# Kernel optimization log

Measured on AMD Instinct MI355X. Metric: run time of the kernel, lower is better.

Reference implementation:

```python
import jax, jax.numpy as jnp
import numpy as np

# normalize2mom(relu): scale so E[act(x)^2] = 1 for x ~ N(0,1). For relu E[relu(x)^2] = 1/2.
ACT_SCALE = 2.0 ** 0.5


def setup_inputs() -> dict:
    key = jax.random.key(0)
    k1, k2, k3 = jax.random.split(key, 3)
    B = 512
    NA, NB = 48, 24          # na = round(2*aspect_ratio*res), nb = 2*res, res=12, ar=2
    DIM = 680                # sum_{l=0}^{7} (2l+1)^2
    features = jax.random.normal(k1, (B, DIM), dtype=jnp.float32)
    D = jax.random.normal(k2, (NA, NB, NA, DIM), dtype=jnp.float32)  # fixed Wigner-D basis buffer
    qw = jax.random.uniform(k3, (NB,), dtype=jnp.float32)            # quadrature weights over beta
    return {"features": features, "D": D, "qw": qw}


def reference(features, D, qw):
    # features: (N, i); D: (a, b, c, i); qw: (b,)
    dim = D.shape[-1]
    inv_sqrt_dim = dim ** -0.5
    # forward SO(3) transform to grid: (N, a, b, c)
    g = jnp.einsum('ni,abci->nabc', features, D) * inv_sqrt_dim
    # pointwise activation (normalized to unit second moment)
    g = ACT_SCALE * jax.nn.relu(g)
    # inverse transform with quadrature weights on the beta axis: (N, i)
    out = jnp.einsum('nabc,abci,b->ni', g, D, qw) * (dim ** 0.5)
    return out
```

## Files before the change

kernel.cpp:

```cpp
#include <hip/hip_runtime.h>

#define BATCH 512
#define SDIM  680
#define DIP   768
#define ABC   55296
#define NB_   24
#define SQRT2F 1.4142135623730951f

typedef __attribute__((ext_vector_type(8))) short bf16x8;
typedef __attribute__((ext_vector_type(4))) float f32x4;

#define DP_BYTES   ((size_t)ABC * DIP * 2)
#define DPT_BYTES  ((size_t)DIP * ABC * 2)
#define FP_BYTES   ((size_t)BATCH * DIP * 2)
#define G_BYTES    ((size_t)BATCH * ABC * 2)
#define DP_OFF     ((size_t)0)
#define DPT_OFF    (DP_OFF + DP_BYTES)
#define FP_OFF     (DPT_OFF + DPT_BYTES)
#define G_OFF      (FP_OFF + FP_BYTES)
#define WS_NEEDED  (G_OFF + G_BYTES)

#define SPLITK 32
#define KC     1728
#define P_OFF  DP_OFF

__device__ __forceinline__ unsigned short f2bf(float f) {
  unsigned int u = __float_as_uint(f);
  unsigned int r = (u + 0x7FFFu + ((u >> 16) & 1u)) >> 16;
  return (unsigned short)r;
}

__device__ __forceinline__ float bf2f(unsigned int bits16) {
  return __uint_as_float(bits16 << 16);
}

__device__ __forceinline__ void stage16(const void* g, const void* l) {
  __builtin_amdgcn_global_load_lds(
      (const __attribute__((address_space(1))) unsigned int*)g,
      (__attribute__((address_space(3))) unsigned int*)l, 16, 0, 0);
}

#define CBP 264
__global__ __launch_bounds__(256) void conv_both(const float* __restrict__ D,
                                                 unsigned short* __restrict__ Dp,
                                                 unsigned short* __restrict__ DpT) {
  __shared__ unsigned short T[64 * CBP];
  const int bid = blockIdx.x;
  const int logical = (bid & 7) * 324 + (bid >> 3);
  const int bx = logical / 12;
  const int by = logical % 12;
  const int t = threadIdx.x;

  #pragma unroll
  for (int k = 0; k < 4; ++k) {
    const int micro = t + k * 256;
    const int r4 = micro >> 4;
    const int c4 = micro & 15;
    const int gr = bx * 256 + r4 * 4;
    const int gi = by * 64 + c4 * 4;
    float4 v[4];
    const bool valid = gi < SDIM;
    #pragma unroll
    for (int dr = 0; dr < 4; ++dr)
      v[dr] = valid ? *(const float4*)(D + (size_t)(gr + dr) * SDIM + gi)
                    : make_float4(0.f, 0.f, 0.f, 0.f);
    const float* fv = reinterpret_cast<const float*>(v);
    #pragma unroll
    for (int dr = 0; dr < 4; ++dr) {
      ushort4 p;
      p.x = f2bf(fv[dr * 4 + 0]); p.y = f2bf(fv[dr * 4 + 1]);
      p.z = f2bf(fv[dr * 4 + 2]); p.w = f2bf(fv[dr * 4 + 3]);
      *(ushort4*)(Dp + (size_t)(gr + dr) * DIP + gi) = p;
    }
    #pragma unroll
    for (int j = 0; j < 4; ++j) {
      ushort4 p;
      p.x = f2bf(fv[0 * 4 + j]); p.y = f2bf(fv[1 * 4 + j]);
      p.z = f2bf(fv[2 * 4 + j]); p.w = f2bf(fv[3 * 4 + j]);
      *(ushort4*)&T[(c4 * 4 + j) * CBP + r4 * 4] = p;
    }
  }
  __syncthreads();
  #pragma unroll
  for (int k = 0; k < 8; ++k) {
    const int v2 = t + k * 256;
    const int c = v2 >> 5;
    const int u = v2 & 31;
    const uint4 q = *(const uint4*)&T[c * CBP + u * 8];
    *(uint4*)(DpT + (size_t)(by * 64 + c) * ABC + bx * 256 + u * 8) = q;
  }
}

__global__ __launch_bounds__(256) void convert_f(const float* __restrict__ F,
                                                 unsigned short* __restrict__ Fp) {
  const int u = blockIdx.x * 256 + threadIdx.x;
  if (u >= BATCH * (DIP / 8)) return;
  const int n = u / (DIP / 8), s = u % (DIP / 8);
  const int i = s * 8;
  float4 a = make_float4(0.f, 0.f, 0.f, 0.f), b = a;
  if (i < SDIM) {
    a = *(const float4*)(F + (size_t)n * SDIM + i);
    b = *(const float4*)(F + (size_t)n * SDIM + i + 4);
  }
  uint4 p;
  p.x = f2bf(a.x) | ((unsigned int)f2bf(a.y) << 16);
  p.y = f2bf(a.z) | ((unsigned int)f2bf(a.w) << 16);
  p.z = f2bf(b.x) | ((unsigned int)f2bf(b.y) << 16);
  p.w = f2bf(b.z) | ((unsigned int)f2bf(b.w) << 16);
  *(uint4*)(Fp + (size_t)n * DIP + i) = p;
}

__global__ __launch_bounds__(512, 1) void gemm1(const unsigned short* __restrict__ Fp,
                                                const unsigned short* __restrict__ Dp,
                                                const float* __restrict__ qw,
                                                unsigned short* __restrict__ G) {
  __shared__ short LDS_[65536];
  __shared__ float qws[NB_];
  short* Ab0 = LDS_;
  short* Bb0 = LDS_ + 32768;
  const int t = threadIdx.x;
  const int bid = blockIdx.x;
  const int logical = (bid & 7) * 54 + (bid >> 3);
  const int nt = logical >> 1, mt = logical & 1;
  const int m0 = mt * 256, n0 = nt * 256;
  if (t < NB_) qws[t] = qw[t] * SQRT2F;

  const int row0 = t >> 3;
  const int scol = ((t & 7) ^ (row0 & 7)) * 8;
  const unsigned short* Asrc = Fp + (size_t)(m0 + row0) * DIP + scol;
  const unsigned short* Bsrc = Dp + (size_t)(n0 + row0) * DIP + scol;

  const int lane = t & 63, wid = t >> 6;
  const int wm = wid >> 2, wn = wid & 3;
  const int fr = lane & 15, fk = lane >> 4;
  const int slotL0 = ((fk) ^ (fr & 7)) * 8;
  const int slotL1 = ((4 + fk) ^ (fr & 7)) * 8;

  f32x4 acc[8][4];
  #pragma unroll
  for (int i = 0; i < 8; ++i)
    #pragma unroll
    for (int j = 0; j < 4; ++j)
      #pragma unroll
      for (int k = 0; k < 4; ++k) acc[i][j][k] = 0.f;

  auto stage = [&](int b, int kt) {
    const unsigned short* ga = Asrc + kt * 64;
    const unsigned short* gb = Bsrc + kt * 64;
    short* la = Ab0 + b * 16384;
    short* lb = Bb0 + b * 16384;
    #pragma unroll
    for (int j = 0; j < 4; ++j) {
      stage16(ga + (size_t)j * 64 * DIP, la + (j * 512 + t) * 8);
      stage16(gb + (size_t)j * 64 * DIP, lb + (j * 512 + t) * 8);
    }
  };

  stage(0, 0);
  const int KT = DIP / 64;
  for (int kt = 0; kt < KT; ++kt) {
    asm volatile("s_waitcnt vmcnt(0)" ::: "memory");
    __builtin_amdgcn_s_barrier();
    if (kt + 1 < KT) stage((kt + 1) & 1, kt + 1);
    const short* At = Ab0 + (kt & 1) * 16384;
    const short* Bt = Bb0 + (kt & 1) * 16384;
    #pragma unroll
    for (int ks = 0; ks < 2; ++ks) {
      const int slot = ks ? slotL1 : slotL0;
      bf16x8 bv[4], av[8];
      #pragma unroll
      for (int ni = 0; ni < 4; ++ni)
        bv[ni] = *(const bf16x8*)&Bt[(wn * 64 + ni * 16 + fr) * 64 + slot];
      #pragma unroll
      for (int mi = 0; mi < 8; ++mi)
        av[mi] = *(const bf16x8*)&At[(wm * 128 + mi * 16 + fr) * 64 + slot];
      __builtin_amdgcn_s_setprio(1);
      #pragma unroll
      for (int mi = 0; mi < 8; ++mi)
        #pragma unroll
        for (int ni = 0; ni < 4; ++ni)
          acc[mi][ni] = __builtin_amdgcn_mfma_f32_16x16x32_bf16(av[mi], bv[ni], acc[mi][ni], 0, 0, 0);
      __builtin_amdgcn_s_setprio(0);
    }
  }

  __syncthreads();
  #pragma unroll
  for (int mi = 0; mi < 8; ++mi) {
    const int row = wm * 128 + mi * 16 + fk * 4;
    #pragma unroll
    for (int ni = 0; ni < 4; ++ni) {
      const int colL = wn * 64 + ni * 16 + fr;
      const float qv = qws[((n0 + colL) / 48) % NB_];
      #pragma unroll
      for (int r = 0; r < 4; ++r)
        LDS_[(row + r) * 256 + colL] = (short)f2bf(fmaxf(acc[mi][ni][r], 0.f) * qv);
    }
  }
  __syncthreads();
  {
    const int row = t >> 1, h = t & 1;
    const unsigned short* src = (const unsigned short*)&LDS_[row * 256 + h * 128];
    unsigned short* dst = G + (size_t)(m0 + row) * ABC + n0 + h * 128;
    #pragma unroll
    for (int c = 0; c < 16; ++c)
      *(uint4*)(dst + c * 8) = *(const uint4*)(src + c * 8);
  }
}

__global__ __launch_bounds__(512, 1) void gemm2(const unsigned short* __restrict__ Gm,
                                                const unsigned short* __restrict__ DpT,
                                                unsigned short* __restrict__ P) {
  __shared__ short LDS_[57344];
  short* Ab0 = LDS_;
  short* Bb0 = LDS_ + 32768;
  const int t = threadIdx.x;
  const int bid = blockIdx.x;
  const int logical = (bid & 7) * 32 + (bid >> 3);
  const int sk = logical >> 3;
  const int rem = logical & 7;
  const int mt = rem >> 2, nt2 = rem & 3;
  const int m0 = mt * 256, n0 = nt2 * 192;
  const size_t kbase = (size_t)sk * KC;

  const int row0 = t >> 3;
  const int scol = ((t & 7) ^ (row0 & 7)) * 8;
  const unsigned short* Asrc = Gm  + (size_t)(m0 + row0) * ABC + kbase + scol;
  const unsigned short* Bsrc = DpT + (size_t)(n0 + row0) * ABC + kbase + scol;

  const int lane = t & 63, wid = t >> 6;
  const int wm = wid >> 2, wn = wid & 3;
  const int fr = lane & 15, fk = lane >> 4;
  const int slotL0 = ((fk) ^ (fr & 7)) * 8;
  const int slotL1 = ((4 + fk) ^ (fr & 7)) * 8;

  f32x4 acc[8][3];
  #pragma unroll
  for (int i = 0; i < 8; ++i)
    #pragma unroll
    for (int j = 0; j < 3; ++j)
      #pragma unroll
      for (int k = 0; k < 4; ++k) acc[i][j][k] = 0.f;

  auto stage = [&](int b, int kt) {
    const unsigned short* ga = Asrc + kt * 64;
    const unsigned short* gb = Bsrc + kt * 64;
    short* la = Ab0 + b * 16384;
    short* lb = Bb0 + b * 12288;
    #pragma unroll
    for (int j = 0; j < 4; ++j)
      stage16(ga + (size_t)j * 64 * ABC, la + (j * 512 + t) * 8);
    #pragma unroll
    for (int j = 0; j < 3; ++j)
      stage16(gb + (size_t)j * 64 * ABC, lb + (j * 512 + t) * 8);
  };

  stage(0, 0);
  const int KT = KC / 64;
  for (int kt = 0; kt < KT; ++kt) {
    asm volatile("s_waitcnt vmcnt(0)" ::: "memory");
    __builtin_amdgcn_s_barrier();
    if (kt + 1 < KT) stage((kt + 1) & 1, kt + 1);
    const short* At = Ab0 + (kt & 1) * 16384;
    const short* Bt = Bb0 + (kt & 1) * 12288;
    #pragma unroll
    for (int ks = 0; ks < 2; ++ks) {
      const int slot = ks ? slotL1 : slotL0;
      bf16x8 bv[3], av[8];
      #pragma unroll
      for (int ni = 0; ni < 3; ++ni)
        bv[ni] = *(const bf16x8*)&Bt[(wn * 48 + ni * 16 + fr) * 64 + slot];
      #pragma unroll
      for (int mi = 0; mi < 8; ++mi)
        av[mi] = *(const bf16x8*)&At[(wm * 128 + mi * 16 + fr) * 64 + slot];
      __builtin_amdgcn_s_setprio(1);
      #pragma unroll
      for (int mi = 0; mi < 8; ++mi)
        #pragma unroll
        for (int ni = 0; ni < 3; ++ni)
          acc[mi][ni] = __builtin_amdgcn_mfma_f32_16x16x32_bf16(av[mi], bv[ni], acc[mi][ni], 0, 0, 0);
      __builtin_amdgcn_s_setprio(0);
    }
  }

  __syncthreads();
  #pragma unroll
  for (int mi = 0; mi < 8; ++mi) {
    const int row = wm * 128 + mi * 16 + fk * 4;
    #pragma unroll
    for (int ni = 0; ni < 3; ++ni) {
      const int colL = wn * 48 + ni * 16 + fr;
      #pragma unroll
      for (int r = 0; r < 4; ++r)
        LDS_[(row + r) * 192 + colL] = (short)f2bf(acc[mi][ni][r]);
    }
  }
  __syncthreads();
  {
    const int row = t >> 1, h = t & 1;
    const unsigned short* src = (const unsigned short*)&LDS_[row * 192 + h * 96];
    unsigned short* dst = P + (size_t)sk * BATCH * DIP +
                          (size_t)(m0 + row) * DIP + n0 + h * 96;
    #pragma unroll
    for (int c = 0; c < 12; ++c)
      *(uint4*)(dst + c * 8) = *(const uint4*)(src + c * 8);
  }
}

__global__ __launch_bounds__(256) void reduce_p(const unsigned short* __restrict__ P,
                                                float* __restrict__ out) {
  const int u = blockIdx.x * 256 + threadIdx.x;
  const int n = u / (SDIM / 4), q = u % (SDIM / 4);
  const int i = q * 4;
  const unsigned short* base = P + (size_t)n * DIP + i;
  const size_t stride = (size_t)BATCH * DIP;
  float s0 = 0.f, s1 = 0.f, s2 = 0.f, s3 = 0.f;
  #pragma unroll 4
  for (int s = 0; s < SPLITK; ++s) {
    const uint2 v = *(const uint2*)(base + (size_t)s * stride);
    s0 += bf2f(v.x & 0xffffu);
    s1 += __uint_as_float(v.x & 0xffff0000u);
    s2 += bf2f(v.y & 0xffffu);
    s3 += __uint_as_float(v.y & 0xffff0000u);
  }
  float4 r; r.x = s0; r.y = s1; r.z = s2; r.w = s3;
  *(float4*)(out + (size_t)n * SDIM + i) = r;
}

__global__ __launch_bounds__(256) void so3_fallback(const float* __restrict__ F,
                                                    const float* __restrict__ D,
                                                    const float* __restrict__ qw,
                                                    float* __restrict__ out) {
  const int n = blockIdx.x;
  __shared__ float fsh[SDIM];
  __shared__ float acc[SDIM];
  __shared__ float gch[256];
  for (int i = threadIdx.x; i < SDIM; i += 256) {
    fsh[i] = F[(size_t)n * SDIM + i];
    acc[i] = 0.f;
  }
  __syncthreads();
  for (int c0 = 0; c0 < ABC; c0 += 256) {
    const int r = c0 + threadIdx.x;
    const float* dr = D + (size_t)r * SDIM;
    float s = 0.f;
    for (int i = 0; i < SDIM; ++i) s += fsh[i] * dr[i];
    s = fmaxf(s, 0.f) * SQRT2F * qw[(r / 48) % NB_];
    gch[threadIdx.x] = s;
    __syncthreads();
    for (int i = threadIdx.x; i < SDIM; i += 256) {
      float a = 0.f;
      for (int tt = 0; tt < 256; ++tt) a += gch[tt] * D[(size_t)(c0 + tt) * SDIM + i];
      acc[i] += a;
    }
    __syncthreads();
  }
  for (int i = threadIdx.x; i < SDIM; i += 256) out[(size_t)n * SDIM + i] = acc[i];
}

extern "C" void kernel_launch(void* const* d_in, const int* in_sizes, int n_in,
                              void* d_out, int out_size, void* d_ws, size_t ws_size,
                              hipStream_t stream) {
  const float* F  = (const float*)d_in[0];
  const float* D  = (const float*)d_in[1];
  const float* qw = (const float*)d_in[2];
  float* out = (float*)d_out;

  if (ws_size < WS_NEEDED) {
    so3_fallback<<<BATCH, 256, 0, stream>>>(F, D, qw, out);
    return;
  }

  unsigned short* Dp  = (unsigned short*)((char*)d_ws + DP_OFF);
  unsigned short* DpT = (unsigned short*)((char*)d_ws + DPT_OFF);
  unsigned short* Fp  = (unsigned short*)((char*)d_ws + FP_OFF);
  unsigned short* G   = (unsigned short*)((char*)d_ws + G_OFF);
  unsigned short* P   = (unsigned short*)((char*)d_ws + P_OFF);

  conv_both<<<2592, 256, 0, stream>>>(D, Dp, DpT);
  convert_f<<<192, 256, 0, stream>>>(F, Fp);
  gemm1<<<432, 512, 0, stream>>>(Fp, Dp, qw, G);
  gemm2<<<256, 512, 0, stream>>>(G, DpT, P);
  reduce_p<<<340, 256, 0, stream>>>(P, out);
}
```

Baseline: 186.4 us.

## Fuse fp32-to-bf16 conversion of D into gemm1 B-tile staging

Removes the separate Dp bf16 copy of D; gemm1 now loads fp32 D directly, converts to bf16 in registers, and writes swizzled tiles into LDS. The conversion kernel now only produces the transposed DpT and runs after gemm1. This saves writing and rereading the Dp buffer, but gemm1 reads twice as many bytes for B, and the B path loses the asynchronous direct-to-LDS loads, which may expose load latency.

```diff
diff --git a/kernel.cpp b/kernel.cpp
--- a/kernel.cpp
+++ b/kernel.cpp
@@ -41,9 +41,8 @@
 }
 
 #define CBP 264
-__global__ __launch_bounds__(256) void conv_both(const float* __restrict__ D,
-                                                 unsigned short* __restrict__ Dp,
-                                                 unsigned short* __restrict__ DpT) {
+__global__ __launch_bounds__(256) void conv_dpt(const float* __restrict__ D,
+                                                unsigned short* __restrict__ DpT) {
   __shared__ unsigned short T[64 * CBP];
   const int bid = blockIdx.x;
   const int logical = (bid & 7) * 324 + (bid >> 3);
@@ -65,13 +64,6 @@
       v[dr] = valid ? *(const float4*)(D + (size_t)(gr + dr) * SDIM + gi)
                     : make_float4(0.f, 0.f, 0.f, 0.f);
     const float* fv = reinterpret_cast<const float*>(v);
-    #pragma unroll
-    for (int dr = 0; dr < 4; ++dr) {
-      ushort4 p;
-      p.x = f2bf(fv[dr * 4 + 0]); p.y = f2bf(fv[dr * 4 + 1]);
-      p.z = f2bf(fv[dr * 4 + 2]); p.w = f2bf(fv[dr * 4 + 3]);
-      *(ushort4*)(Dp + (size_t)(gr + dr) * DIP + gi) = p;
-    }
     #pragma unroll
     for (int j = 0; j < 4; ++j) {
       ushort4 p;
@@ -111,7 +103,7 @@
 }
 
 __global__ __launch_bounds__(512, 1) void gemm1(const unsigned short* __restrict__ Fp,
-                                                const unsigned short* __restrict__ Dp,
+                                                const float* __restrict__ D,
                                                 const float* __restrict__ qw,
                                                 unsigned short* __restrict__ G) {
   __shared__ short LDS_[65536];
@@ -128,7 +120,6 @@
   const int row0 = t >> 3;
   const int scol = ((t & 7) ^ (row0 & 7)) * 8;
   const unsigned short* Asrc = Fp + (size_t)(m0 + row0) * DIP + scol;
-  const unsigned short* Bsrc = Dp + (size_t)(n0 + row0) * DIP + scol;
 
   const int lane = t & 63, wid = t >> 6;
   const int wm = wid >> 2, wn = wid & 3;
@@ -144,24 +135,42 @@
       #pragma unroll
       for (int k = 0; k < 4; ++k) acc[i][j][k] = 0.f;
 
-  auto stage = [&](int b, int kt) {
+  auto stageA = [&](int b, int kt) {
     const unsigned short* ga = Asrc + kt * 64;
-    const unsigned short* gb = Bsrc + kt * 64;
     short* la = Ab0 + b * 16384;
+    #pragma unroll
+    for (int j = 0; j < 4; ++j)
+      stage16(ga + (size_t)j * 64 * DIP, la + (j * 512 + t) * 8);
+  };
+  auto stageB = [&](int b, int kt) {
     short* lb = Bb0 + b * 16384;
     #pragma unroll
     for (int j = 0; j < 4; ++j) {
-      stage16(ga + (size_t)j * 64 * DIP, la + (j * 512 + t) * 8);
-      stage16(gb + (size_t)j * 64 * DIP, lb + (j * 512 + t) * 8);
+      const int u = t + j * 512;
+      const int row = u >> 3;
+      const int k8 = u & 7;
+      const int gi = kt * 64 + k8 * 8;
+      float4 a = make_float4(0.f, 0.f, 0.f, 0.f), c = a;
+      if (gi < SDIM) {
+        const float* src = D + (size_t)(n0 + row) * SDIM + gi;
+        a = *(const float4*)(src);
+        c = *(const float4*)(src + 4);
+      }
+      bf16x8 h;
+      h[0] = (short)f2bf(a.x); h[1] = (short)f2bf(a.y);
+      h[2] = (short)f2bf(a.z); h[3] = (short)f2bf(a.w);
+      h[4] = (short)f2bf(c.x); h[5] = (short)f2bf(c.y);
+      h[6] = (short)f2bf(c.z); h[7] = (short)f2bf(c.w);
+      *(bf16x8*)&lb[row * 64 + (k8 ^ (row & 7)) * 8] = h;
     }
   };
 
-  stage(0, 0);
+  stageA(0, 0); stageB(0, 0);
   const int KT = DIP / 64;
   for (int kt = 0; kt < KT; ++kt) {
-    asm volatile("s_waitcnt vmcnt(0)" ::: "memory");
+    asm volatile("s_waitcnt vmcnt(0) lgkmcnt(0)" ::: "memory");
     __builtin_amdgcn_s_barrier();
-    if (kt + 1 < KT) stage((kt + 1) & 1, kt + 1);
+    if (kt + 1 < KT) { stageA((kt + 1) & 1, kt + 1); stageB((kt + 1) & 1, kt + 1); }
     const short* At = Ab0 + (kt & 1) * 16384;
     const short* Bt = Bb0 + (kt & 1) * 16384;
     #pragma unroll
@@ -371,15 +380,14 @@
     return;
   }
 
-  unsigned short* Dp  = (unsigned short*)((char*)d_ws + DP_OFF);
   unsigned short* DpT = (unsigned short*)((char*)d_ws + DPT_OFF);
   unsigned short* Fp  = (unsigned short*)((char*)d_ws + FP_OFF);
   unsigned short* G   = (unsigned short*)((char*)d_ws + G_OFF);
   unsigned short* P   = (unsigned short*)((char*)d_ws + P_OFF);
 
-  conv_both<<<2592, 256, 0, stream>>>(D, Dp, DpT);
   convert_f<<<192, 256, 0, stream>>>(F, Fp);
-  gemm1<<<432, 512, 0, stream>>>(Fp, Dp, qw, G);
+  gemm1<<<432, 512, 0, stream>>>(Fp, D, qw, G);
+  conv_dpt<<<2592, 256, 0, stream>>>(D, DpT);
   gemm2<<<256, 512, 0, stream>>>(G, DpT, P);
   reduce_p<<<340, 256, 0, stream>>>(P, out);
 }
```

Result: slower. 221.1 us (+18.6%).
